# Optimization experiments

Measured on AMD Instinct MI355X. Metric: run time of the kernel, lower is better.

Reference implementation:

```python
import jax, jax.numpy as jnp
import numpy as np

D = 128  # node_dim (hardcoded in the torch module)


def _bn(x, g, b, eps=1e-5):
    # BatchNorm1d in training mode: per-batch mean / biased variance
    m = x.mean(0)
    v = x.var(0)
    return (x - m) * jax.lax.rsqrt(v + eps) * g + b


def setup_inputs() -> dict:
    key = jax.random.key(0)
    ks = jax.random.split(key, 16)
    N, E, ED = 4096, 16384, 16
    node = jax.random.normal(ks[0], (N, D), jnp.float32)
    edge = jax.random.normal(ks[1], (E, ED), jnp.float32)
    hidden = jax.random.normal(ks[2], (1, N, D), jnp.float32)
    edge_index = jax.random.randint(ks[3], (E, 2), 0, N)

    def lin(k, o, i):
        return jax.random.normal(k, (o, i), jnp.float32) / np.sqrt(i).astype(np.float32)

    W1 = lin(ks[4], 256, ED)
    W2 = lin(ks[5], 256, 256)
    W3 = lin(ks[6], 128, 256)
    W4 = lin(ks[7], D * D, 128)
    g1, b1 = jnp.ones(256), jnp.zeros(256)
    g2, b2 = jnp.ones(256), jnp.zeros(256)
    g3, b3 = jnp.ones(128), jnp.zeros(128)
    g4, b4 = jnp.ones(D * D), jnp.zeros(D * D)
    lim = 1.0 / np.sqrt(D).astype(np.float32)
    bias = jax.random.uniform(ks[8], (D,), jnp.float32, -lim, lim)
    W_ih = lin(ks[9], 3 * D, D)
    W_hh = lin(ks[10], 3 * D, D)
    b_ih = jnp.zeros(3 * D)
    b_hh = jnp.zeros(3 * D)
    return dict(node=node, edge_index=edge_index, edge=edge, hidden=hidden,
                W1=W1, g1=g1, b1=b1, W2=W2, g2=g2, b2=b2, W3=W3, g3=g3, b3=b3,
                W4=W4, g4=g4, b4=b4, bias=bias, W_ih=W_ih, W_hh=W_hh,
                b_ih=b_ih, b_hh=b_hh)


def reference(node, edge_index, edge, hidden, W1, g1, b1, W2, g2, b2,
              W3, g3, b3, W4, g4, b4, bias, W_ih, W_hh, b_ih, b_hh):
    N = node.shape[0]
    E = edge.shape[0]
    h0 = hidden[0]  # [N, D]
    src, dst = edge_index[:, 0], edge_index[:, 1]

    # edge encoder -> per-edge [D, D] weight matrix
    x = jax.nn.relu(_bn(edge @ W1.T, g1, b1))
    x = jax.nn.relu(_bn(x @ W2.T, g2, b2))
    x = jax.nn.relu(_bn(x @ W3.T, g3, b3))
    w = _bn(x @ W4.T, g4, b4).reshape(E, D, D)

    # gather source nodes, per-edge vector-matrix product
    x_i = node[src]                               # [E, D]
    msg = jnp.einsum('ed,edk->ek', x_i, w)        # [E, D]

    # scatter-mean over destination nodes
    sums = jax.ops.segment_sum(msg, dst, num_segments=N)
    cnt = jax.ops.segment_sum(jnp.ones((E, 1), msg.dtype), dst, num_segments=N)
    message = sums / jnp.maximum(cnt, 1.0)
    m = jax.nn.relu(message + bias)               # [N, D]

    # single-step GRU (PyTorch gate order r, z, n)
    gi = m @ W_ih.T + b_ih
    gh = h0 @ W_hh.T + b_hh
    r = jax.nn.sigmoid(gi[:, :D] + gh[:, :D])
    z = jax.nn.sigmoid(gi[:, D:2 * D] + gh[:, D:2 * D])
    n = jnp.tanh(gi[:, 2 * D:] + r * gh[:, 2 * D:])
    hn = (1.0 - z) * n + z * h0                   # [N, D]
    return hn, hn[None]
```

## Files before the change

### kernel.cpp

```cpp
#include <hip/hip_runtime.h>

#define EPS 1e-5f

typedef _Float16 half8 __attribute__((ext_vector_type(8)));
typedef float f32x16 __attribute__((ext_vector_type(16)));

__device__ __forceinline__ float dot4(float4 a, float4 b) {
  return a.x * b.x + a.y * b.y + a.z * b.z + a.w * b.w;
}

__global__ __launch_bounds__(256) void gemm_abt(const float* __restrict__ A,
                                                const float* __restrict__ B,
                                                float* __restrict__ C,
                                                int M, int N, int K,
                                                float* __restrict__ osum,
                                                float* __restrict__ osq) {
  __shared__ float As[16][68];
  __shared__ float Bs[16][68];
  const int t = threadIdx.x;
  const int tx = t & 15, ty = t >> 4;
  const int m0 = blockIdx.y * 64, n0 = blockIdx.x * 64;
  float acc[4][4] = {};
  for (int k0 = 0; k0 < K; k0 += 16) {
    __syncthreads();
    {
      const int r = t >> 2;
      const int kk = (t & 3) << 2;
      float4 av = *(const float4*)&A[(size_t)(m0 + r) * K + k0 + kk];
      As[kk + 0][r] = av.x; As[kk + 1][r] = av.y;
      As[kk + 2][r] = av.z; As[kk + 3][r] = av.w;
      float4 bv = *(const float4*)&B[(size_t)(n0 + r) * K + k0 + kk];
      Bs[kk + 0][r] = bv.x; Bs[kk + 1][r] = bv.y;
      Bs[kk + 2][r] = bv.z; Bs[kk + 3][r] = bv.w;
    }
    __syncthreads();
#pragma unroll
    for (int kk = 0; kk < 16; ++kk) {
      float4 a = *(const float4*)&As[kk][ty << 2];
      float4 b = *(const float4*)&Bs[kk][tx << 2];
      float av[4] = {a.x, a.y, a.z, a.w};
      float bv[4] = {b.x, b.y, b.z, b.w};
#pragma unroll
      for (int i = 0; i < 4; ++i)
#pragma unroll
        for (int j = 0; j < 4; ++j) acc[i][j] += av[i] * bv[j];
    }
  }
#pragma unroll
  for (int i = 0; i < 4; ++i) {
    float4 o = make_float4(acc[i][0], acc[i][1], acc[i][2], acc[i][3]);
    *(float4*)&C[(size_t)(m0 + (ty << 2) + i) * N + n0 + (tx << 2)] = o;
  }
  __syncthreads();
  float* sred = (float*)As;
  if (t < 128) sred[t] = 0.f;
  __syncthreads();
#pragma unroll
  for (int j = 0; j < 4; ++j) {
    float s = 0.f, sq = 0.f;
#pragma unroll
    for (int i = 0; i < 4; ++i) {
      float v = acc[i][j];
      s += v; sq += v * v;
    }
    atomicAdd(&sred[((tx << 2) + j) * 2 + 0], s);
    atomicAdd(&sred[((tx << 2) + j) * 2 + 1], sq);
  }
  __syncthreads();
  if (t < 64) {
    atomicAdd(&osum[n0 + t], sred[t * 2]);
    atomicAdd(&osq[n0 + t], sred[t * 2 + 1]);
  }
}

template <int TRANS, bool STATS>
__global__ __launch_bounds__(256) void gemm16(const float* __restrict__ A,
                                              const float* __restrict__ B,
                                              float* __restrict__ C,
                                              int lda, int ldb, int ldc, int K,
                                              const float* __restrict__ s1,
                                              const float* __restrict__ s2,
                                              const float* __restrict__ g,
                                              const float* __restrict__ b,
                                              float invM,
                                              float* __restrict__ osum,
                                              float* __restrict__ osq) {
  __shared__ _Float16 As[128 * 64];
  __shared__ _Float16 Bs[128 * 64];
  __shared__ float scL[256], shL[256];
  const int t = threadIdx.x;
  const int m0 = blockIdx.y * 128, n0 = blockIdx.x * 128;
  const int w = t >> 6, l = t & 63;
  const int wm = w >> 1, wn = w & 1;
  const int lr = l & 31, lg = l >> 5;
  if (TRANS == 1) {
    if (t < K) {
      float mean = s1[t] * invM;
      float var = s2[t] * invM - mean * mean;
      float sc = g[t] * rsqrtf(var + EPS);
      scL[t] = sc;
      shL[t] = b[t] - mean * sc;
    }
  }
  f32x16 acc[2][2];
#pragma unroll
  for (int i = 0; i < 2; ++i)
#pragma unroll
    for (int j = 0; j < 2; ++j) acc[i][j] = (f32x16){0.f};
  for (int k0 = 0; k0 < K; k0 += 64) {
    __syncthreads();
#pragma unroll
    for (int i = 0; i < 4; ++i) {
      const int gq = i * 256 + t;
      const int f = gq >> 6, lp = gq & 63;
      const int row = (f >> 2) * 32 + (lp & 31);
      const int c = (f & 3) * 16 + (lp >> 5) * 8;
      const float* ap = A + (size_t)(m0 + row) * lda + k0 + c;
      float4 a4 = *(const float4*)ap, b4 = *(const float4*)(ap + 4);
      float va[8] = {a4.x, a4.y, a4.z, a4.w, b4.x, b4.y, b4.z, b4.w};
      if (TRANS == 1) {
#pragma unroll
        for (int j = 0; j < 8; ++j)
          va[j] = fmaxf(va[j] * scL[k0 + c + j] + shL[k0 + c + j], 0.f);
      } else if (TRANS == 2) {
        float rc = 1.f / fmaxf(s1[m0 + row], 1.f);
#pragma unroll
        for (int j = 0; j < 8; ++j) va[j] = fmaxf(va[j] * rc + s2[k0 + c + j], 0.f);
      }
      half8 h;
#pragma unroll
      for (int j = 0; j < 8; ++j) h[j] = (_Float16)va[j];
      *(half8*)(As + (size_t)gq * 8) = h;
      const float* bp = B + (size_t)(n0 + row) * ldb + k0 + c;
      float4 e4 = *(const float4*)bp, f4 = *(const float4*)(bp + 4);
      half8 hb;
      hb[0] = (_Float16)e4.x; hb[1] = (_Float16)e4.y; hb[2] = (_Float16)e4.z; hb[3] = (_Float16)e4.w;
      hb[4] = (_Float16)f4.x; hb[5] = (_Float16)f4.y; hb[6] = (_Float16)f4.z; hb[7] = (_Float16)f4.w;
      *(half8*)(Bs + (size_t)gq * 8) = hb;
    }
    __syncthreads();
#pragma unroll
    for (int ks = 0; ks < 4; ++ks) {
      half8 af[2], bf[2];
#pragma unroll
      for (int mb = 0; mb < 2; ++mb) {
        const int fa = ((wm * 2 + mb) * 4 + ks);
        af[mb] = *(const half8*)(As + (size_t)(fa * 64 + l) * 8);
        const int fb = ((wn * 2 + mb) * 4 + ks);
        bf[mb] = *(const half8*)(Bs + (size_t)(fb * 64 + l) * 8);
      }
#pragma unroll
      for (int mb = 0; mb < 2; ++mb)
#pragma unroll
        for (int nb = 0; nb < 2; ++nb)
          acc[mb][nb] = __builtin_amdgcn_mfma_f32_32x32x16_f16(af[mb], bf[nb], acc[mb][nb], 0, 0, 0);
    }
  }
#pragma unroll
  for (int mb = 0; mb < 2; ++mb)
#pragma unroll
    for (int nb = 0; nb < 2; ++nb)
#pragma unroll
      for (int r = 0; r < 16; ++r) {
        const int row = m0 + wm * 64 + mb * 32 + (r & 3) + 8 * (r >> 2) + 4 * lg;
        const int col = n0 + wn * 64 + nb * 32 + lr;
        C[(size_t)row * ldc + col] = acc[mb][nb][r];
      }
  if (STATS) {
    __syncthreads();
    float* sred = (float*)As;
    if (t < 256) sred[t] = 0.f;
    __syncthreads();
#pragma unroll
    for (int nb = 0; nb < 2; ++nb) {
      float s = 0.f, sq = 0.f;
#pragma unroll
      for (int mb = 0; mb < 2; ++mb)
#pragma unroll
        for (int r = 0; r < 16; ++r) {
          float v = acc[mb][nb][r];
          s += v; sq += v * v;
        }
      const int cl = wn * 64 + nb * 32 + lr;
      atomicAdd(&sred[cl * 2 + 0], s);
      atomicAdd(&sred[cl * 2 + 1], sq);
    }
    __syncthreads();
    if (t < 128) {
      atomicAdd(&osum[n0 + t], sred[t * 2]);
      atomicAdd(&osq[n0 + t], sred[t * 2 + 1]);
    }
  }
}

__global__ __launch_bounds__(256) void bn_apply(float* __restrict__ y,
                                                const float* __restrict__ colsum,
                                                const float* __restrict__ colsumsq,
                                                const float* __restrict__ g,
                                                const float* __restrict__ b,
                                                int M, int N) {
  const int idx = blockIdx.x * 256 + threadIdx.x;
  const int col = idx % N;
  const float invM = 1.0f / (float)M;
  float mean = colsum[col] * invM;
  float var = colsumsq[col] * invM - mean * mean;
  float v = (y[idx] - mean) * rsqrtf(var + EPS) * g[col] + b[col];
  y[idx] = fmaxf(v, 0.f);
}

__global__ __launch_bounds__(256) void gram_kernel(const float* __restrict__ x,
                                                   float* __restrict__ part, int M) {
  __shared__ float xL[128 * 132];
  const int t = threadIdx.x, tx = t & 15, ty = t >> 4;
  float acc[8][8] = {};
  float csum[8] = {};
  const int rpb = M / gridDim.x;
  for (int r0 = blockIdx.x * rpb; r0 < blockIdx.x * rpb + rpb; r0 += 128) {
    __syncthreads();
#pragma unroll
    for (int i = 0; i < 16; ++i) {
      int f4 = t + i * 256;
      int r = f4 >> 5;
      int c4 = (f4 & 31) << 2;
      *(float4*)&xL[r * 132 + c4] = *(const float4*)&x[(size_t)(r0 + r) * 128 + c4];
    }
    __syncthreads();
    for (int r = 0; r < 128; ++r) {
      float4 a0 = *(const float4*)&xL[r * 132 + ty * 8];
      float4 a1 = *(const float4*)&xL[r * 132 + ty * 8 + 4];
      float4 b0 = *(const float4*)&xL[r * 132 + tx * 8];
      float4 b1 = *(const float4*)&xL[r * 132 + tx * 8 + 4];
      float a[8] = {a0.x, a0.y, a0.z, a0.w, a1.x, a1.y, a1.z, a1.w};
      float b[8] = {b0.x, b0.y, b0.z, b0.w, b1.x, b1.y, b1.z, b1.w};
#pragma unroll
      for (int i = 0; i < 8; ++i)
#pragma unroll
        for (int j = 0; j < 8; ++j) acc[i][j] += a[i] * b[j];
      if (tx == ty) {
#pragma unroll
        for (int i = 0; i < 8; ++i) csum[i] += a[i];
      }
    }
  }
  float* base = part + (size_t)blockIdx.x * 16512;
#pragma unroll
  for (int i = 0; i < 8; ++i)
#pragma unroll
    for (int j = 0; j < 8; ++j)
      base[(ty * 8 + i) * 128 + tx * 8 + j] = acc[i][j];
  if (tx == ty) {
#pragma unroll
    for (int i = 0; i < 8; ++i) base[16384 + ty * 8 + i] = csum[i];
  }
}

__global__ __launch_bounds__(256) void gram_reduce(const float* __restrict__ part,
                                                   float* __restrict__ out) {
  int idx = blockIdx.x * 256 + threadIdx.x;
  if (idx >= 16512) return;
  float s = 0.f;
  for (int b = 0; b < 128; ++b) s += part[(size_t)b * 16512 + idx];
  out[idx] = s;
}

__global__ __launch_bounds__(256) void w4_finalize(const float* __restrict__ W4,
                                                   const float* __restrict__ U,
                                                   const float* __restrict__ colsum3,
                                                   const float* __restrict__ g4,
                                                   const float* __restrict__ b4,
                                                   _Float16* __restrict__ BTf,
                                                   float* __restrict__ t4,
                                                   float invM) {
  const int r = (blockIdx.x * 256 + threadIdx.x) >> 6;
  const int lane = threadIdx.x & 63;
  const float* wp = W4 + (size_t)r * 128;
  const float* up = U + (size_t)r * 128;
  float p1 = 0.f, p2 = 0.f;
#pragma unroll
  for (int c0 = 0; c0 < 128; c0 += 64) {
    float wv = wp[c0 + lane];
    p1 += up[c0 + lane] * wv;
    p2 += colsum3[c0 + lane] * wv;
  }
#pragma unroll
  for (int off = 32; off > 0; off >>= 1) {
    p1 += __shfl_down(p1, off);
    p2 += __shfl_down(p2, off);
  }
  p1 = __shfl(p1, 0);
  p2 = __shfl(p2, 0);
  float m4 = p2 * invM;
  float q = p1 * invM;
  float s = g4[r] * rsqrtf(q - m4 * m4 + EPS);
  if (lane == 0) t4[r] = b4[r] - m4 * s;
  const int kout = r & 127, d = r >> 7;
  if (lane < 16) {
    const int ks = lane >> 1, lg = lane & 1;
    const float* cp = wp + lane * 8;
    float4 va = *(const float4*)cp, vb = *(const float4*)(cp + 4);
    half8 h;
    h[0] = (_Float16)(s * va.x); h[1] = (_Float16)(s * va.y);
    h[2] = (_Float16)(s * va.z); h[3] = (_Float16)(s * va.w);
    h[4] = (_Float16)(s * vb.x); h[5] = (_Float16)(s * vb.y);
    h[6] = (_Float16)(s * vb.z); h[7] = (_Float16)(s * vb.w);
    size_t off16 = (size_t)d * 16384 +
                   (size_t)((((kout >> 5) * 8 + ks) * 64) + (kout & 31) + lg * 32) * 8;
    *(half8*)(BTf + off16) = h;
  }
}

__global__ __launch_bounds__(256, 2) void zgemm(const float* __restrict__ x3,
                                                const float* __restrict__ node,
                                                const int* __restrict__ eidx,
                                                const _Float16* __restrict__ BTf,
                                                const float* __restrict__ Tn,
                                                float* __restrict__ sums) {
  __shared__ _Float16 Bs[2][16384];
  __shared__ _Float16 xiL[32 * 128];
  const int t = threadIdx.x;
  const int e0 = blockIdx.y * 128;
  const int d0 = blockIdx.x * 32;
  const int w = t >> 6, l = t & 63;
  const int wm = w >> 1, wn = w & 1;
  const int lr = l & 31, lg = l >> 5;
  {
    const int e = t >> 1, db = (t & 1) * 16;
    const int src = eidx[(e0 + e) * 2];
    const float* np = node + (size_t)src * 128 + d0 + db;
#pragma unroll
    for (int j = 0; j < 16; j += 4) {
      float4 v = *(const float4*)(np + j);
      xiL[(db + j + 0) * 128 + e] = (_Float16)v.x;
      xiL[(db + j + 1) * 128 + e] = (_Float16)v.y;
      xiL[(db + j + 2) * 128 + e] = (_Float16)v.z;
      xiL[(db + j + 3) * 128 + e] = (_Float16)v.w;
    }
  }
  half8 xf[2][8];
#pragma unroll
  for (int mb = 0; mb < 2; ++mb) {
    const float* xp = x3 + (size_t)(e0 + wm * 64 + mb * 32 + lr) * 128 + lg * 8;
#pragma unroll
    for (int ks = 0; ks < 8; ++ks) {
      float4 a = *(const float4*)(xp + ks * 16);
      float4 b = *(const float4*)(xp + ks * 16 + 4);
      half8 h;
      h[0] = (_Float16)a.x; h[1] = (_Float16)a.y; h[2] = (_Float16)a.z; h[3] = (_Float16)a.w;
      h[4] = (_Float16)b.x; h[5] = (_Float16)b.y; h[6] = (_Float16)b.z; h[7] = (_Float16)b.w;
      xf[mb][ks] = h;
    }
  }
  f32x16 acc00 = (f32x16){0.f}, acc01 = (f32x16){0.f};
  f32x16 acc10 = (f32x16){0.f}, acc11 = (f32x16){0.f};
  half8 st[8];
  {
    const _Float16* p = BTf + (size_t)d0 * 16384 + (size_t)t * 8;
#pragma unroll
    for (int j = 0; j < 8; ++j) st[j] = *(const half8*)(p + j * 2048);
  }
  __syncthreads();
  for (int dt = 0; dt < 32; ++dt) {
    _Float16* bs = &Bs[dt & 1][0];
#pragma unroll
    for (int j = 0; j < 8; ++j) *(half8*)(bs + t * 8 + j * 2048) = st[j];
    if (dt < 31) {
      const _Float16* p = BTf + (size_t)(d0 + dt + 1) * 16384 + (size_t)t * 8;
#pragma unroll
      for (int j = 0; j < 8; ++j) st[j] = *(const half8*)(p + j * 2048);
    }
    asm volatile("s_waitcnt lgkmcnt(0)" ::: "memory");
    __builtin_amdgcn_s_barrier();
    const _Float16 xv0 = xiL[dt * 128 + wm * 64 + lr];
    const _Float16 xv1 = xiL[dt * 128 + wm * 64 + 32 + lr];
    const half8 xb0 = {xv0, xv0, xv0, xv0, xv0, xv0, xv0, xv0};
    const half8 xb1 = {xv1, xv1, xv1, xv1, xv1, xv1, xv1, xv1};
#pragma unroll
    for (int ks = 0; ks < 8; ++ks) {
      half8 b0 = *(const half8*)(bs + (size_t)(((wn * 2 + 0) * 8 + ks) * 64 + l) * 8);
      half8 b1 = *(const half8*)(bs + (size_t)(((wn * 2 + 1) * 8 + ks) * 64 + l) * 8);
      half8 a0 = xf[0][ks] * xb0;
      half8 a1 = xf[1][ks] * xb1;
      acc00 = __builtin_amdgcn_mfma_f32_32x32x16_f16(a0, b0, acc00, 0, 0, 0);
      acc01 = __builtin_amdgcn_mfma_f32_32x32x16_f16(a0, b1, acc01, 0, 0, 0);
      acc10 = __builtin_amdgcn_mfma_f32_32x32x16_f16(a1, b0, acc10, 0, 0, 0);
      acc11 = __builtin_amdgcn_mfma_f32_32x32x16_f16(a1, b1, acc11, 0, 0, 0);
    }
  }
  const bool add_t = (blockIdx.x == 0);
#pragma unroll
  for (int r = 0; r < 16; ++r) {
    const int rl = (r & 3) + 8 * (r >> 2) + 4 * lg;
    const int eA = e0 + wm * 64 + rl;
    const int eB = eA + 32;
    const int dA = eidx[eA * 2 + 1], sA = eidx[eA * 2];
    const int dB = eidx[eB * 2 + 1], sB = eidx[eB * 2];
    const int c0 = wn * 64 + lr;
    float v00 = acc00[r], v01 = acc01[r], v10 = acc10[r], v11 = acc11[r];
    if (add_t) {
      v00 += Tn[(size_t)sA * 128 + c0];
      v01 += Tn[(size_t)sA * 128 + c0 + 32];
      v10 += Tn[(size_t)sB * 128 + c0];
      v11 += Tn[(size_t)sB * 128 + c0 + 32];
    }
    atomicAdd(&sums[(size_t)dA * 128 + c0], v00);
    atomicAdd(&sums[(size_t)dA * 128 + c0 + 32], v01);
    atomicAdd(&sums[(size_t)dB * 128 + c0], v10);
    atomicAdd(&sums[(size_t)dB * 128 + c0 + 32], v11);
  }
}

__global__ __launch_bounds__(128) void t4n_kernel(const float* __restrict__ node,
                                                  const float* __restrict__ t4,
                                                  float* __restrict__ Tn) {
  __shared__ float nodeL[8][128];
  const int k = threadIdx.x;
  const int n0 = blockIdx.x * 8;
#pragma unroll
  for (int j = 0; j < 8; ++j) nodeL[j][k] = node[(size_t)(n0 + j) * 128 + k];
  __syncthreads();
  float acc[8] = {};
  for (int d = 0; d < 128; ++d) {
    float wv = t4[d * 128 + k];
#pragma unroll
    for (int j = 0; j < 8; ++j) acc[j] += nodeL[j][d] * wv;
  }
#pragma unroll
  for (int j = 0; j < 8; ++j) Tn[(size_t)(n0 + j) * 128 + k] = acc[j];
}

__global__ __launch_bounds__(256) void cnt_kernel(const int* __restrict__ eidx,
                                                  float* __restrict__ cnt, int E) {
  int e = blockIdx.x * 256 + threadIdx.x;
  if (e < E) atomicAdd(&cnt[eidx[e * 2 + 1]], 1.0f);
}

__global__ __launch_bounds__(256) void gru_gates(const float* __restrict__ sums,
                                                 const float* __restrict__ cnt,
                                                 const float* __restrict__ bias,
                                                 const float* __restrict__ h0,
                                                 const float* __restrict__ Wih,
                                                 const float* __restrict__ Whh,
                                                 float* __restrict__ gi,
                                                 float* __restrict__ gh) {
  __shared__ _Float16 As[128 * 64];
  __shared__ _Float16 Bs[128 * 64];
  const bool isgh = blockIdx.x >= 3;
  const float* A = isgh ? h0 : sums;
  const float* B = isgh ? Whh : Wih;
  float* C = isgh ? gh : gi;
  const int n0 = (isgh ? blockIdx.x - 3 : blockIdx.x) * 128;
  const int m0 = blockIdx.y * 128;
  const int t = threadIdx.x;
  const int w = t >> 6, l = t & 63;
  const int wm = w >> 1, wn = w & 1;
  const int lr = l & 31, lg = l >> 5;
  f32x16 acc[2][2];
#pragma unroll
  for (int i = 0; i < 2; ++i)
#pragma unroll
    for (int j = 0; j < 2; ++j) acc[i][j] = (f32x16){0.f};
  for (int k0 = 0; k0 < 128; k0 += 64) {
    __syncthreads();
#pragma unroll
    for (int i = 0; i < 4; ++i) {
      const int gq = i * 256 + t;
      const int f = gq >> 6, lp = gq & 63;
      const int row = (f >> 2) * 32 + (lp & 31);
      const int c = (f & 3) * 16 + (lp >> 5) * 8;
      const float* ap = A + (size_t)(m0 + row) * 128 + k0 + c;
      float4 a4 = *(const float4*)ap, b4 = *(const float4*)(ap + 4);
      float va[8] = {a4.x, a4.y, a4.z, a4.w, b4.x, b4.y, b4.z, b4.w};
      if (!isgh) {
        float rc = 1.f / fmaxf(cnt[m0 + row], 1.f);
#pragma unroll
        for (int j = 0; j < 8; ++j) va[j] = fmaxf(va[j] * rc + bias[k0 + c + j], 0.f);
      }
      half8 h;
#pragma unroll
      for (int j = 0; j < 8; ++j) h[j] = (_Float16)va[j];
      *(half8*)(As + (size_t)gq * 8) = h;
      const float* bp = B + (size_t)(n0 + row) * 128 + k0 + c;
      float4 e4 = *(const float4*)bp, f4 = *(const float4*)(bp + 4);
      half8 hb;
      hb[0] = (_Float16)e4.x; hb[1] = (_Float16)e4.y; hb[2] = (_Float16)e4.z; hb[3] = (_Float16)e4.w;
      hb[4] = (_Float16)f4.x; hb[5] = (_Float16)f4.y; hb[6] = (_Float16)f4.z; hb[7] = (_Float16)f4.w;
      *(half8*)(Bs + (size_t)gq * 8) = hb;
    }
    __syncthreads();
#pragma unroll
    for (int ks = 0; ks < 4; ++ks) {
      half8 af[2], bf[2];
#pragma unroll
      for (int mb = 0; mb < 2; ++mb) {
        af[mb] = *(const half8*)(As + (size_t)(((wm * 2 + mb) * 4 + ks) * 64 + l) * 8);
        bf[mb] = *(const half8*)(Bs + (size_t)(((wn * 2 + mb) * 4 + ks) * 64 + l) * 8);
      }
#pragma unroll
      for (int mb = 0; mb < 2; ++mb)
#pragma unroll
        for (int nb = 0; nb < 2; ++nb)
          acc[mb][nb] = __builtin_amdgcn_mfma_f32_32x32x16_f16(af[mb], bf[nb], acc[mb][nb], 0, 0, 0);
    }
  }
#pragma unroll
  for (int mb = 0; mb < 2; ++mb)
#pragma unroll
    for (int nb = 0; nb < 2; ++nb)
#pragma unroll
      for (int r = 0; r < 16; ++r) {
        const int row = m0 + wm * 64 + mb * 32 + (r & 3) + 8 * (r >> 2) + 4 * lg;
        const int col = n0 + wn * 64 + nb * 32 + lr;
        C[(size_t)row * 384 + col] = acc[mb][nb][r];
      }
}

__global__ __launch_bounds__(256) void gru_finalize(const float* __restrict__ gi,
                                                    const float* __restrict__ gh,
                                                    const float* __restrict__ h0,
                                                    const float* __restrict__ bih,
                                                    const float* __restrict__ bhh,
                                                    float* __restrict__ out, int Nn) {
  int idx = blockIdx.x * 256 + threadIdx.x;
  int n = idx >> 7, k = idx & 127;
  const float* gin = gi + (size_t)n * 384;
  const float* ghn = gh + (size_t)n * 384;
  float r = 1.f / (1.f + expf(-(gin[k] + bih[k] + ghn[k] + bhh[k])));
  float z = 1.f / (1.f + expf(-(gin[128 + k] + bih[128 + k] + ghn[128 + k] + bhh[128 + k])));
  float nn = tanhf(gin[256 + k] + bih[256 + k] + r * (ghn[256 + k] + bhh[256 + k]));
  float h = h0[idx];
  float hn = (1.f - z) * nn + z * h;
  out[idx] = hn;
  out[idx + (size_t)Nn * 128] = hn;
}

extern "C" void kernel_launch(void* const* d_in, const int* in_sizes, int n_in,
                              void* d_out, int out_size, void* d_ws, size_t ws_size,
                              hipStream_t stream) {
  const float* node = (const float*)d_in[0];
  const int* eidx = (const int*)d_in[1];
  const float* edge = (const float*)d_in[2];
  const float* hidden = (const float*)d_in[3];
  const float* W1 = (const float*)d_in[4];
  const float* g1 = (const float*)d_in[5];
  const float* b1 = (const float*)d_in[6];
  const float* W2 = (const float*)d_in[7];
  const float* g2 = (const float*)d_in[8];
  const float* b2 = (const float*)d_in[9];
  const float* W3 = (const float*)d_in[10];
  const float* g3 = (const float*)d_in[11];
  const float* b3 = (const float*)d_in[12];
  const float* W4 = (const float*)d_in[13];
  const float* g4 = (const float*)d_in[14];
  const float* b4 = (const float*)d_in[15];
  const float* bias = (const float*)d_in[16];
  const float* Wih = (const float*)d_in[17];
  const float* Whh = (const float*)d_in[18];
  const float* bih = (const float*)d_in[19];
  const float* bhh = (const float*)d_in[20];
  float* out = (float*)d_out;

  const int Nn = in_sizes[0] / 128;
  const int E = in_sizes[2] / 16;
  const float invE = 1.0f / (float)E;

  float* ws = (float*)d_ws;
  float* ybuf1 = ws + 0;
  float* ybuf2 = ws + 4194304;
  float* x3 = ws + 8388608;
  _Float16* BTf = (_Float16*)(ws + 10485760);
  float* t4 = ws + 11534336;
  float* stats = ws + 11550720;
  float* G3 = ws + 11552256;
  float* sums = ws + 11568768;
  float* cnt = ws + 12093056;
  float* Tn = ws + 12097152;
  float* stat1 = stats, *stat2 = stats + 512, *stat3 = stats + 1024;
  float* gpart = ybuf1;
  float* U = ybuf2;
  float* gi = ybuf2;
  float* gh = ybuf2 + 1572864;

  hipMemsetAsync(stats, 0, 1536 * sizeof(float), stream);

  gemm_abt<<<dim3(4, E / 64), 256, 0, stream>>>(edge, W1, ybuf1, E, 256, 16, stat1, stat1 + 256);
  gemm16<1, true><<<dim3(2, E / 128), 256, 0, stream>>>(ybuf1, W2, ybuf2, 256, 256, 256, 256,
                                                        stat1, stat1 + 256, g1, b1, invE,
                                                        stat2, stat2 + 256);
  gemm16<1, true><<<dim3(1, E / 128), 256, 0, stream>>>(ybuf2, W3, x3, 256, 256, 128, 256,
                                                        stat2, stat2 + 256, g2, b2, invE,
                                                        stat3, stat3 + 256);
  bn_apply<<<E * 128 / 256, 256, 0, stream>>>(x3, stat3, stat3 + 256, g3, b3, E, 128);

  gram_kernel<<<128, 256, 0, stream>>>(x3, gpart, E);
  gram_reduce<<<65, 256, 0, stream>>>(gpart, G3);

  gemm16<0, false><<<dim3(1, 16384 / 128), 256, 0, stream>>>(W4, G3, U, 128, 128, 128, 128,
                                                             nullptr, nullptr, nullptr, nullptr,
                                                             0.f, nullptr, nullptr);
  w4_finalize<<<16384 / 4, 256, 0, stream>>>(W4, U, G3 + 16384, g4, b4, BTf, t4, invE);
  t4n_kernel<<<Nn / 8, 128, 0, stream>>>(node, t4, Tn);

  hipMemsetAsync(sums, 0, ((size_t)Nn * 128 + Nn) * sizeof(float), stream);
  cnt_kernel<<<(E + 255) / 256, 256, 0, stream>>>(eidx, cnt, E);
  zgemm<<<dim3(4, E / 128), 256, 0, stream>>>(x3, node, eidx, BTf, Tn, sums);

  gru_gates<<<dim3(6, Nn / 128), 256, 0, stream>>>(sums, cnt, bias, hidden, Wih, Whh, gi, gh);
  gru_finalize<<<Nn * 128 / 256, 256, 0, stream>>>(gi, gh, hidden, bih, bhh, out, Nn);
}
```

Baseline: 235.8 us.

## Fuse BN3 into gram and zgemm, async LDS loads, restructure zgemm warp tiling

Removes the standalone bn_apply pass by recomputing the layer-3 BatchNorm scale/shift inside gram_kernel and zgemm and applying it on load. gram_kernel now runs one 64-row tile per block over more blocks, and accumulates column sums through atomics instead of writing them as partials. zgemm loads BT tiles with global_load_lds straight into shared memory instead of staging through registers, and each warp now covers all 128 edges for a 32-column slice. In exchange, the BN arithmetic is recomputed in two kernels, gram_reduce reduces over twice as many partials, and zgemm holds more register state.

New measurement: 308.4 us. 30.8% more time.

```diff
diff --git a/kernel.cpp b/kernel.cpp
--- a/kernel.cpp
+++ b/kernel.cpp
@@ -5,8 +5,9 @@
 typedef _Float16 half8 __attribute__((ext_vector_type(8)));
 typedef float f32x16 __attribute__((ext_vector_type(16)));
 
-__device__ __forceinline__ float dot4(float4 a, float4 b) {
-  return a.x * b.x + a.y * b.y + a.z * b.z + a.w * b.w;
+__device__ __forceinline__ void gload16(const void* g, void* l) {
+  __builtin_amdgcn_global_load_lds((const __attribute__((address_space(1))) void*)g,
+                                   (__attribute__((address_space(3))) void*)l, 16, 0, 0);
 }
 
 __global__ __launch_bounds__(256) void gemm_abt(const float* __restrict__ A,
@@ -122,10 +123,6 @@
 #pragma unroll
         for (int j = 0; j < 8; ++j)
           va[j] = fmaxf(va[j] * scL[k0 + c + j] + shL[k0 + c + j], 0.f);
-      } else if (TRANS == 2) {
-        float rc = 1.f / fmaxf(s1[m0 + row], 1.f);
-#pragma unroll
-        for (int j = 0; j < 8; ++j) va[j] = fmaxf(va[j] * rc + s2[k0 + c + j], 0.f);
       }
       half8 h;
 #pragma unroll
@@ -144,10 +141,8 @@
       half8 af[2], bf[2];
 #pragma unroll
       for (int mb = 0; mb < 2; ++mb) {
-        const int fa = ((wm * 2 + mb) * 4 + ks);
-        af[mb] = *(const half8*)(As + (size_t)(fa * 64 + l) * 8);
-        const int fb = ((wn * 2 + mb) * 4 + ks);
-        bf[mb] = *(const half8*)(Bs + (size_t)(fb * 64 + l) * 8);
+        af[mb] = *(const half8*)(As + (size_t)(((wm * 2 + mb) * 4 + ks) * 64 + l) * 8);
+        bf[mb] = *(const half8*)(Bs + (size_t)(((wn * 2 + mb) * 4 + ks) * 64 + l) * 8);
       }
 #pragma unroll
       for (int mb = 0; mb < 2; ++mb)
@@ -193,56 +188,58 @@
   }
 }
 
-__global__ __launch_bounds__(256) void bn_apply(float* __restrict__ y,
-                                                const float* __restrict__ colsum,
-                                                const float* __restrict__ colsumsq,
-                                                const float* __restrict__ g,
-                                                const float* __restrict__ b,
-                                                int M, int N) {
-  const int idx = blockIdx.x * 256 + threadIdx.x;
-  const int col = idx % N;
-  const float invM = 1.0f / (float)M;
-  float mean = colsum[col] * invM;
-  float var = colsumsq[col] * invM - mean * mean;
-  float v = (y[idx] - mean) * rsqrtf(var + EPS) * g[col] + b[col];
-  y[idx] = fmaxf(v, 0.f);
-}
-
-__global__ __launch_bounds__(256) void gram_kernel(const float* __restrict__ x,
-                                                   float* __restrict__ part, int M) {
-  __shared__ float xL[128 * 132];
+__global__ __launch_bounds__(256) void gram_kernel(const float* __restrict__ y3,
+                                                   float* __restrict__ part,
+                                                   const float* __restrict__ s3sum,
+                                                   const float* __restrict__ s3sq,
+                                                   const float* __restrict__ g3,
+                                                   const float* __restrict__ b3,
+                                                   float invE,
+                                                   float* __restrict__ colsum) {
+  __shared__ float xL[64 * 132];
+  __shared__ float scL[128], shL[128];
   const int t = threadIdx.x, tx = t & 15, ty = t >> 4;
+  if (t < 128) {
+    float mean = s3sum[t] * invE;
+    float var = s3sq[t] * invE - mean * mean;
+    float sc = g3[t] * rsqrtf(var + EPS);
+    scL[t] = sc;
+    shL[t] = b3[t] - mean * sc;
+  }
+  __syncthreads();
+  const int r0 = blockIdx.x * 64;
+#pragma unroll
+  for (int i = 0; i < 8; ++i) {
+    int f4 = t + i * 256;
+    int r = f4 >> 5;
+    int c4 = (f4 & 31) << 2;
+    float4 v = *(const float4*)&y3[(size_t)(r0 + r) * 128 + c4];
+    v.x = fmaxf(v.x * scL[c4 + 0] + shL[c4 + 0], 0.f);
+    v.y = fmaxf(v.y * scL[c4 + 1] + shL[c4 + 1], 0.f);
+    v.z = fmaxf(v.z * scL[c4 + 2] + shL[c4 + 2], 0.f);
+    v.w = fmaxf(v.w * scL[c4 + 3] + shL[c4 + 3], 0.f);
+    *(float4*)&xL[r * 132 + c4] = v;
+  }
+  __syncthreads();
   float acc[8][8] = {};
   float csum[8] = {};
-  const int rpb = M / gridDim.x;
-  for (int r0 = blockIdx.x * rpb; r0 < blockIdx.x * rpb + rpb; r0 += 128) {
-    __syncthreads();
-#pragma unroll
-    for (int i = 0; i < 16; ++i) {
-      int f4 = t + i * 256;
-      int r = f4 >> 5;
-      int c4 = (f4 & 31) << 2;
-      *(float4*)&xL[r * 132 + c4] = *(const float4*)&x[(size_t)(r0 + r) * 128 + c4];
-    }
-    __syncthreads();
-    for (int r = 0; r < 128; ++r) {
-      float4 a0 = *(const float4*)&xL[r * 132 + ty * 8];
-      float4 a1 = *(const float4*)&xL[r * 132 + ty * 8 + 4];
-      float4 b0 = *(const float4*)&xL[r * 132 + tx * 8];
-      float4 b1 = *(const float4*)&xL[r * 132 + tx * 8 + 4];
-      float a[8] = {a0.x, a0.y, a0.z, a0.w, a1.x, a1.y, a1.z, a1.w};
-      float b[8] = {b0.x, b0.y, b0.z, b0.w, b1.x, b1.y, b1.z, b1.w};
-#pragma unroll
-      for (int i = 0; i < 8; ++i)
-#pragma unroll
-        for (int j = 0; j < 8; ++j) acc[i][j] += a[i] * b[j];
-      if (tx == ty) {
-#pragma unroll
-        for (int i = 0; i < 8; ++i) csum[i] += a[i];
-      }
-    }
-  }
-  float* base = part + (size_t)blockIdx.x * 16512;
+  for (int r = 0; r < 64; ++r) {
+    float4 a0 = *(const float4*)&xL[r * 132 + ty * 8];
+    float4 a1 = *(const float4*)&xL[r * 132 + ty * 8 + 4];
+    float4 b0 = *(const float4*)&xL[r * 132 + tx * 8];
+    float4 b1 = *(const float4*)&xL[r * 132 + tx * 8 + 4];
+    float a[8] = {a0.x, a0.y, a0.z, a0.w, a1.x, a1.y, a1.z, a1.w};
+    float b[8] = {b0.x, b0.y, b0.z, b0.w, b1.x, b1.y, b1.z, b1.w};
+#pragma unroll
+    for (int i = 0; i < 8; ++i)
+#pragma unroll
+      for (int j = 0; j < 8; ++j) acc[i][j] += a[i] * b[j];
+    if (tx == ty) {
+#pragma unroll
+      for (int i = 0; i < 8; ++i) csum[i] += a[i];
+    }
+  }
+  float* base = part + (size_t)blockIdx.x * 16384;
 #pragma unroll
   for (int i = 0; i < 8; ++i)
 #pragma unroll
@@ -250,16 +247,15 @@
       base[(ty * 8 + i) * 128 + tx * 8 + j] = acc[i][j];
   if (tx == ty) {
 #pragma unroll
-    for (int i = 0; i < 8; ++i) base[16384 + ty * 8 + i] = csum[i];
+    for (int i = 0; i < 8; ++i) atomicAdd(&colsum[ty * 8 + i], csum[i]);
   }
 }
 
 __global__ __launch_bounds__(256) void gram_reduce(const float* __restrict__ part,
                                                    float* __restrict__ out) {
   int idx = blockIdx.x * 256 + threadIdx.x;
-  if (idx >= 16512) return;
   float s = 0.f;
-  for (int b = 0; b < 128; ++b) s += part[(size_t)b * 16512 + idx];
+  for (int b = 0; b < 256; ++b) s += part[(size_t)b * 16384 + idx];
   out[idx] = s;
 }
 
@@ -309,20 +305,32 @@
   }
 }
 
-__global__ __launch_bounds__(256, 2) void zgemm(const float* __restrict__ x3,
+__global__ __launch_bounds__(256, 2) void zgemm(const float* __restrict__ y3,
                                                 const float* __restrict__ node,
                                                 const int* __restrict__ eidx,
                                                 const _Float16* __restrict__ BTf,
                                                 const float* __restrict__ Tn,
+                                                const float* __restrict__ s3sum,
+                                                const float* __restrict__ s3sq,
+                                                const float* __restrict__ g3,
+                                                const float* __restrict__ b3,
+                                                float invE,
                                                 float* __restrict__ sums) {
-  __shared__ _Float16 Bs[2][16384];
+  __shared__ __align__(16) _Float16 Bs[2][16384];
   __shared__ _Float16 xiL[32 * 128];
+  __shared__ float scL[128], shL[128];
   const int t = threadIdx.x;
   const int e0 = blockIdx.y * 128;
   const int d0 = blockIdx.x * 32;
   const int w = t >> 6, l = t & 63;
-  const int wm = w >> 1, wn = w & 1;
   const int lr = l & 31, lg = l >> 5;
+  if (t < 128) {
+    float mean = s3sum[t] * invE;
+    float var = s3sq[t] * invE - mean * mean;
+    float sc = g3[t] * rsqrtf(var + EPS);
+    scL[t] = sc;
+    shL[t] = b3[t] - mean * sc;
+  }
   {
     const int e = t >> 1, db = (t & 1) * 16;
     const int src = eidx[(e0 + e) * 2];
@@ -336,77 +344,70 @@
       xiL[(db + j + 3) * 128 + e] = (_Float16)v.w;
     }
   }
-  half8 xf[2][8];
-#pragma unroll
-  for (int mb = 0; mb < 2; ++mb) {
-    const float* xp = x3 + (size_t)(e0 + wm * 64 + mb * 32 + lr) * 128 + lg * 8;
+  {
+    const _Float16* gsrc = BTf + (size_t)d0 * 16384 + w * 4096;
+    _Float16* ldst = &Bs[0][w * 4096];
+#pragma unroll
+    for (int j = 0; j < 8; ++j) gload16(gsrc + j * 512 + l * 8, ldst + j * 512);
+  }
+  __syncthreads();
+  half8 xf[4][8];
+#pragma unroll
+  for (int mb = 0; mb < 4; ++mb) {
+    const float* xp = y3 + (size_t)(e0 + mb * 32 + lr) * 128 + lg * 8;
 #pragma unroll
     for (int ks = 0; ks < 8; ++ks) {
+      const int c = ks * 16 + lg * 8;
       float4 a = *(const float4*)(xp + ks * 16);
       float4 b = *(const float4*)(xp + ks * 16 + 4);
+      float va[8] = {a.x, a.y, a.z, a.w, b.x, b.y, b.z, b.w};
       half8 h;
-      h[0] = (_Float16)a.x; h[1] = (_Float16)a.y; h[2] = (_Float16)a.z; h[3] = (_Float16)a.w;
-      h[4] = (_Float16)b.x; h[5] = (_Float16)b.y; h[6] = (_Float16)b.z; h[7] = (_Float16)b.w;
+#pragma unroll
+      for (int j = 0; j < 8; ++j)
+        h[j] = (_Float16)fmaxf(va[j] * scL[c + j] + shL[c + j], 0.f);
       xf[mb][ks] = h;
     }
   }
-  f32x16 acc00 = (f32x16){0.f}, acc01 = (f32x16){0.f};
-  f32x16 acc10 = (f32x16){0.f}, acc11 = (f32x16){0.f};
-  half8 st[8];
-  {
-    const _Float16* p = BTf + (size_t)d0 * 16384 + (size_t)t * 8;
-#pragma unroll
-    for (int j = 0; j < 8; ++j) st[j] = *(const half8*)(p + j * 2048);
-  }
-  __syncthreads();
+  f32x16 acc[4];
+#pragma unroll
+  for (int i = 0; i < 4; ++i) acc[i] = (f32x16){0.f};
+
   for (int dt = 0; dt < 32; ++dt) {
-    _Float16* bs = &Bs[dt & 1][0];
-#pragma unroll
-    for (int j = 0; j < 8; ++j) *(half8*)(bs + t * 8 + j * 2048) = st[j];
+    asm volatile("s_waitcnt vmcnt(0)" ::: "memory");
+    __builtin_amdgcn_s_barrier();
+    const _Float16* bs = &Bs[dt & 1][0];
     if (dt < 31) {
-      const _Float16* p = BTf + (size_t)(d0 + dt + 1) * 16384 + (size_t)t * 8;
-#pragma unroll
-      for (int j = 0; j < 8; ++j) st[j] = *(const half8*)(p + j * 2048);
-    }
-    asm volatile("s_waitcnt lgkmcnt(0)" ::: "memory");
-    __builtin_amdgcn_s_barrier();
-    const _Float16 xv0 = xiL[dt * 128 + wm * 64 + lr];
-    const _Float16 xv1 = xiL[dt * 128 + wm * 64 + 32 + lr];
-    const half8 xb0 = {xv0, xv0, xv0, xv0, xv0, xv0, xv0, xv0};
-    const half8 xb1 = {xv1, xv1, xv1, xv1, xv1, xv1, xv1, xv1};
+      const _Float16* gsrc = BTf + (size_t)(d0 + dt + 1) * 16384 + w * 4096;
+      _Float16* ldst = &Bs[(dt + 1) & 1][w * 4096];
+#pragma unroll
+      for (int j = 0; j < 8; ++j) gload16(gsrc + j * 512 + l * 8, ldst + j * 512);
+    }
+    _Float16 xv[4];
+#pragma unroll
+    for (int mb = 0; mb < 4; ++mb) xv[mb] = xiL[dt * 128 + mb * 32 + lr];
 #pragma unroll
     for (int ks = 0; ks < 8; ++ks) {
-      half8 b0 = *(const half8*)(bs + (size_t)(((wn * 2 + 0) * 8 + ks) * 64 + l) * 8);
-      half8 b1 = *(const half8*)(bs + (size_t)(((wn * 2 + 1) * 8 + ks) * 64 + l) * 8);
-      half8 a0 = xf[0][ks] * xb0;
-      half8 a1 = xf[1][ks] * xb1;
-      acc00 = __builtin_amdgcn_mfma_f32_32x32x16_f16(a0, b0, acc00, 0, 0, 0);
-      acc01 = __builtin_amdgcn_mfma_f32_32x32x16_f16(a0, b1, acc01, 0, 0, 0);
-      acc10 = __builtin_amdgcn_mfma_f32_32x32x16_f16(a1, b0, acc10, 0, 0, 0);
-      acc11 = __builtin_amdgcn_mfma_f32_32x32x16_f16(a1, b1, acc11, 0, 0, 0);
+      half8 bf = *(const half8*)(bs + ((size_t)(w * 8 + ks) * 64 + l) * 8);
+#pragma unroll
+      for (int mb = 0; mb < 4; ++mb) {
+        half8 xb = {xv[mb], xv[mb], xv[mb], xv[mb], xv[mb], xv[mb], xv[mb], xv[mb]};
+        half8 a = xf[mb][ks] * xb;
+        acc[mb] = __builtin_amdgcn_mfma_f32_32x32x16_f16(a, bf, acc[mb], 0, 0, 0);
+      }
     }
   }
   const bool add_t = (blockIdx.x == 0);
-#pragma unroll
-  for (int r = 0; r < 16; ++r) {
-    const int rl = (r & 3) + 8 * (r >> 2) + 4 * lg;
-    const int eA = e0 + wm * 64 + rl;
-    const int eB = eA + 32;
-    const int dA = eidx[eA * 2 + 1], sA = eidx[eA * 2];
-    const int dB = eidx[eB * 2 + 1], sB = eidx[eB * 2];
-    const int c0 = wn * 64 + lr;
-    float v00 = acc00[r], v01 = acc01[r], v10 = acc10[r], v11 = acc11[r];
-    if (add_t) {
-      v00 += Tn[(size_t)sA * 128 + c0];
-      v01 += Tn[(size_t)sA * 128 + c0 + 32];
-      v10 += Tn[(size_t)sB * 128 + c0];
-      v11 += Tn[(size_t)sB * 128 + c0 + 32];
-    }
-    atomicAdd(&sums[(size_t)dA * 128 + c0], v00);
-    atomicAdd(&sums[(size_t)dA * 128 + c0 + 32], v01);
-    atomicAdd(&sums[(size_t)dB * 128 + c0], v10);
-    atomicAdd(&sums[(size_t)dB * 128 + c0 + 32], v11);
-  }
+  const int col = w * 32 + lr;
+#pragma unroll
+  for (int mb = 0; mb < 4; ++mb)
+#pragma unroll
+    for (int r = 0; r < 16; ++r) {
+      const int e = e0 + mb * 32 + (r & 3) + 8 * (r >> 2) + 4 * lg;
+      const int dn = eidx[e * 2 + 1];
+      float v = acc[mb][r];
+      if (add_t) v += Tn[(size_t)eidx[e * 2] * 128 + col];
+      atomicAdd(&sums[(size_t)dn * 128 + col], v);
+    }
 }
 
 __global__ __launch_bounds__(128) void t4n_kernel(const float* __restrict__ node,
@@ -566,43 +567,45 @@
   float* ws = (float*)d_ws;
   float* ybuf1 = ws + 0;
   float* ybuf2 = ws + 4194304;
-  float* x3 = ws + 8388608;
+  float* y3buf = ws + 8388608;
   _Float16* BTf = (_Float16*)(ws + 10485760);
   float* t4 = ws + 11534336;
   float* stats = ws + 11550720;
-  float* G3 = ws + 11552256;
-  float* sums = ws + 11568768;
-  float* cnt = ws + 12093056;
-  float* Tn = ws + 12097152;
+  float* G3 = ws + 11552512;
+  float* sums = ws + 11568896;
+  float* cnt = ws + 12093184;
+  float* Tn = ws + 12097280;
   float* stat1 = stats, *stat2 = stats + 512, *stat3 = stats + 1024;
+  float* colsum3 = stats + 1536;
   float* gpart = ybuf1;
   float* U = ybuf2;
   float* gi = ybuf2;
   float* gh = ybuf2 + 1572864;
 
-  hipMemsetAsync(stats, 0, 1536 * sizeof(float), stream);
+  hipMemsetAsync(stats, 0, 1664 * sizeof(float), stream);
 
   gemm_abt<<<dim3(4, E / 64), 256, 0, stream>>>(edge, W1, ybuf1, E, 256, 16, stat1, stat1 + 256);
   gemm16<1, true><<<dim3(2, E / 128), 256, 0, stream>>>(ybuf1, W2, ybuf2, 256, 256, 256, 256,
                                                         stat1, stat1 + 256, g1, b1, invE,
                                                         stat2, stat2 + 256);
-  gemm16<1, true><<<dim3(1, E / 128), 256, 0, stream>>>(ybuf2, W3, x3, 256, 256, 128, 256,
+  gemm16<1, true><<<dim3(1, E / 128), 256, 0, stream>>>(ybuf2, W3, y3buf, 256, 256, 128, 256,
                                                         stat2, stat2 + 256, g2, b2, invE,
                                                         stat3, stat3 + 256);
-  bn_apply<<<E * 128 / 256, 256, 0, stream>>>(x3, stat3, stat3 + 256, g3, b3, E, 128);
-
-  gram_kernel<<<128, 256, 0, stream>>>(x3, gpart, E);
-  gram_reduce<<<65, 256, 0, stream>>>(gpart, G3);
+
+  gram_kernel<<<E / 64, 256, 0, stream>>>(y3buf, gpart, stat3, stat3 + 256, g3, b3, invE,
+                                          colsum3);
+  gram_reduce<<<64, 256, 0, stream>>>(gpart, G3);
 
   gemm16<0, false><<<dim3(1, 16384 / 128), 256, 0, stream>>>(W4, G3, U, 128, 128, 128, 128,
                                                              nullptr, nullptr, nullptr, nullptr,
                                                              0.f, nullptr, nullptr);
-  w4_finalize<<<16384 / 4, 256, 0, stream>>>(W4, U, G3 + 16384, g4, b4, BTf, t4, invE);
+  w4_finalize<<<16384 / 4, 256, 0, stream>>>(W4, U, colsum3, g4, b4, BTf, t4, invE);
   t4n_kernel<<<Nn / 8, 128, 0, stream>>>(node, t4, Tn);
 
   hipMemsetAsync(sums, 0, ((size_t)Nn * 128 + Nn) * sizeof(float), stream);
   cnt_kernel<<<(E + 255) / 256, 256, 0, stream>>>(eidx, cnt, E);
-  zgemm<<<dim3(4, E / 128), 256, 0, stream>>>(x3, node, eidx, BTf, Tn, sums);
+  zgemm<<<dim3(4, E / 128), 256, 0, stream>>>(y3buf, node, eidx, BTf, Tn,
+                                              stat3, stat3 + 256, g3, b3, invE, sums);
 
   gru_gates<<<dim3(6, Nn / 128), 256, 0, stream>>>(sums, cnt, bias, hidden, Wih, Whh, gi, gh);
   gru_finalize<<<Nn * 128 / 256, 256, 0, stream>>>(gi, gh, hidden, bih, bhh, out, Nn);
```
